# Performance work log

Measured on AMD Instinct MI355X. Metric: run time of the kernel, lower is better.

The kernel has to match this reference:

```python
import jax, jax.numpy as jnp
import numpy as np
from jax import lax

H = 64          # GRU hidden size
OUT_STEPS = 20  # output_seq_size


def _maxpool2(x):
    # x: [N, C, H, W] -> 2x2 max pool, stride 2, VALID
    return lax.reduce_window(x, -jnp.inf, lax.max, (1, 1, 2, 2), (1, 1, 2, 2), 'VALID')


def _conv(x, w, b):
    # NCHW / OIHW, VALID, stride 1
    y = lax.conv_general_dilated(x, w, (1, 1), 'VALID',
                                 dimension_numbers=('NCHW', 'OIHW', 'NCHW'))
    return y + b[None, :, None, None]


def _gru_step(h, x, wih, whh, bih, bhh):
    # PyTorch GRU gate order: r, z, n
    gi = x @ wih.T + bih            # [B, 3H]
    gh = h @ whh.T + bhh            # [B, 3H]
    i_r, i_z, i_n = jnp.split(gi, 3, axis=-1)
    h_r, h_z, h_n = jnp.split(gh, 3, axis=-1)
    r = jax.nn.sigmoid(i_r + h_r)
    z = jax.nn.sigmoid(i_z + h_z)
    n = jnp.tanh(i_n + r * h_n)
    return (1.0 - z) * n + z * h


def setup_inputs() -> dict:
    key = jax.random.key(0)
    ks = jax.random.split(key, 20)
    B, T = 1024, 31
    s = 0.1
    return {
        'bbox_seq': jax.random.normal(ks[0], (B, T, 4), jnp.float32),
        'head_seq': jax.random.uniform(ks[1], (B, T, 32, 32), jnp.float32),
        'conv1_w': jax.random.normal(ks[2], (4, 1, 3, 3), jnp.float32) * s,
        'conv1_b': jax.random.normal(ks[3], (4,), jnp.float32) * s,
        'conv2_w': jax.random.normal(ks[4], (10, 4, 3, 3), jnp.float32) * s,
        'conv2_b': jax.random.normal(ks[5], (10,), jnp.float32) * s,
        'fc_w': jax.random.normal(ks[6], (5, 360), jnp.float32) * s,
        'fc_b': jax.random.normal(ks[7], (5,), jnp.float32) * s,
        'enc_wih': jax.random.normal(ks[8], (3 * H, 9), jnp.float32) * s,
        'enc_whh': jax.random.normal(ks[9], (3 * H, H), jnp.float32) * s,
        'enc_bih': jax.random.normal(ks[10], (3 * H,), jnp.float32) * s,
        'enc_bhh': jax.random.normal(ks[11], (3 * H,), jnp.float32) * s,
        'dec_wih': jax.random.normal(ks[12], (3 * H, 4), jnp.float32) * s,
        'dec_whh': jax.random.normal(ks[13], (3 * H, H), jnp.float32) * s,
        'dec_bih': jax.random.normal(ks[14], (3 * H,), jnp.float32) * s,
        'dec_bhh': jax.random.normal(ks[15], (3 * H,), jnp.float32) * s,
        'lin_w': jax.random.normal(ks[16], (4, H), jnp.float32) * s,
        'lin_b': jax.random.normal(ks[17], (4,), jnp.float32) * s,
    }


def reference(bbox_seq, head_seq, conv1_w, conv1_b, conv2_w, conv2_b, fc_w, fc_b,
              enc_wih, enc_whh, enc_bih, enc_bhh,
              dec_wih, dec_whh, dec_bih, dec_bhh, lin_w, lin_b):
    B, T = bbox_seq.shape[0], bbox_seq.shape[1]
    L = T - 1  # encoder sequence length

    # offset: last bbox, broadcast over OUT_STEPS -> [B, OUT_STEPS, 4]
    offset = jnp.broadcast_to(bbox_seq[:, -1][:, None, :], (B, OUT_STEPS, 4))

    diffs = bbox_seq[:, 1:] - bbox_seq[:, :-1]  # [B, L, 4] (dropout p=0 -> identity)

    # --- ConvEncoder on all head crops at once ---
    imgs = head_seq[:, :-1].reshape(B * L, 1, 32, 32)
    x = jax.nn.relu(_conv(imgs, conv1_w, conv1_b))   # [BL, 4, 30, 30]
    x = _maxpool2(x)                                  # [BL, 4, 15, 15]
    x = jax.nn.relu(_conv(x, conv2_w, conv2_b))       # [BL, 10, 13, 13]
    x = _maxpool2(x)                                  # [BL, 10, 6, 6]
    emb = x.reshape(B * L, -1) @ fc_w.T + fc_b        # [BL, 5]
    emb = emb.reshape(B, L, -1)

    enc_in = jnp.concatenate([diffs, emb], axis=2)    # [B, L, 9]

    # --- GRU encoder (scan over time) ---
    def enc_step(h, x_t):
        h = _gru_step(h, x_t, enc_wih, enc_whh, enc_bih, enc_bhh)
        return h, None
    h0 = jnp.zeros((B, H), enc_in.dtype)
    hn, _ = lax.scan(enc_step, h0, jnp.swapaxes(enc_in, 0, 1))

    def dec_step(carry, _):
        h, prev_x = carry
        h = _gru_step(h, prev_x, dec_wih, dec_whh, dec_bih, dec_bhh)
        x_new = h @ lin_w.T + lin_b + prev_x
        return (h, x_new), x_new
    (_, _), outs = lax.scan(dec_step, (hn, diffs[:, -1]), None, length=OUT_STEPS)
    out = jnp.swapaxes(outs, 0, 1)                    # [B, OUT_STEPS, 4]

    return jnp.cumsum(out, axis=1) + offset
```

## Files before the change

kernel.cpp:

```cpp
#include <hip/hip_runtime.h>
#include <hip/hip_bf16.h>


#define B_    1024
#define L_    30
#define H_    64

__device__ __forceinline__ float sigmoid_f(float v) {
    return 1.f / (1.f + __expf(-v));
}
__device__ __forceinline__ float tanh_f(float v) {
    v = fminf(fmaxf(v, -15.f), 15.f);
    float e = __expf(2.f * v);
    return (e - 1.f) / (e + 1.f);
}
__device__ __forceinline__ void load4_lds(float* r, const float* p) {
    float2 a = *(const float2*)p;
    float2 b = *(const float2*)(p + 2);
    r[0] = a.x; r[1] = a.y; r[2] = b.x; r[3] = b.y;
}

__global__ __launch_bounds__(64) void conv_embed_kernel(
    const float* __restrict__ bbox,
    const float* __restrict__ head,
    const float* __restrict__ c1w, const float* __restrict__ c1b,
    const float* __restrict__ c2w, const float* __restrict__ c2b,
    const float* __restrict__ fcw, const float* __restrict__ fcb,
    float* __restrict__ enc_in)
{
    const int img = blockIdx.x;
    const int b = img / L_;
    const int l = img % L_;
    const int tid = threadIdx.x;

    __shared__ float s_img[32 * 32];
    __shared__ float s_p1[4 * 15 * 16];
    __shared__ float s_p2[360];
    __shared__ float s_red[60];

    {
        const float4* src = (const float4*)(head + ((size_t)b * 31 + (size_t)l) * 1024);
        float4* dst = (float4*)s_img;
        #pragma unroll
        for (int i = 0; i < 4; ++i) dst[tid + 64 * i] = src[tid + 64 * i];
    }
    __syncthreads();

    if (tid < 60) {
        const int c = tid / 15, px = tid % 15;
        const int x0 = 2 * px;
        float w[9];
        #pragma unroll
        for (int k = 0; k < 9; ++k) w[k] = c1w[c * 9 + k];
        const float bias = c1b[c];

        float r0[4], r1[4], r2[4], r3[4];
        load4_lds(r0, s_img + 0 * 32 + x0);
        load4_lds(r1, s_img + 1 * 32 + x0);
        #pragma unroll
        for (int py = 0; py < 15; ++py) {
            load4_lds(r2, s_img + (2 * py + 2) * 32 + x0);
            load4_lds(r3, s_img + (2 * py + 3) * 32 + x0);
            float a00 = bias, a01 = bias, a10 = bias, a11 = bias;
            #pragma unroll
            for (int kx = 0; kx < 3; ++kx) {
                const float w0 = w[kx], w1 = w[3 + kx], w2 = w[6 + kx];
                a00 = fmaf(w0, r0[kx],     fmaf(w1, r1[kx],     fmaf(w2, r2[kx],     a00)));
                a01 = fmaf(w0, r0[kx + 1], fmaf(w1, r1[kx + 1], fmaf(w2, r2[kx + 1], a01)));
                a10 = fmaf(w0, r1[kx],     fmaf(w1, r2[kx],     fmaf(w2, r3[kx],     a10)));
                a11 = fmaf(w0, r1[kx + 1], fmaf(w1, r2[kx + 1], fmaf(w2, r3[kx + 1], a11)));
            }
            a00 = fmaxf(a00, 0.f); a01 = fmaxf(a01, 0.f);
            a10 = fmaxf(a10, 0.f); a11 = fmaxf(a11, 0.f);
            s_p1[c * 240 + py * 16 + px] = fmaxf(fmaxf(a00, a01), fmaxf(a10, a11));
            #pragma unroll
            for (int q = 0; q < 4; ++q) { r0[q] = r2[q]; r1[q] = r3[q]; }
        }
    }
    __syncthreads();

    if (tid < 60) {
        const int c = tid / 6, px = tid % 6;
        const int x0 = 2 * px;
        float w[4][9];
        #pragma unroll
        for (int ic = 0; ic < 4; ++ic)
            #pragma unroll
            for (int k = 0; k < 9; ++k) w[ic][k] = c2w[(c * 4 + ic) * 9 + k];
        const float bias = c2b[c];

        float win[4][4][4];
        #pragma unroll
        for (int ic = 0; ic < 4; ++ic) {
            load4_lds(win[0][ic], s_p1 + ic * 240 + 0 * 16 + x0);
            load4_lds(win[1][ic], s_p1 + ic * 240 + 1 * 16 + x0);
        }
        #pragma unroll
        for (int py = 0; py < 6; ++py) {
            #pragma unroll
            for (int ic = 0; ic < 4; ++ic) {
                load4_lds(win[2][ic], s_p1 + ic * 240 + (2 * py + 2) * 16 + x0);
                load4_lds(win[3][ic], s_p1 + ic * 240 + (2 * py + 3) * 16 + x0);
            }
            float a00 = bias, a01 = bias, a10 = bias, a11 = bias;
            #pragma unroll
            for (int ic = 0; ic < 4; ++ic) {
                #pragma unroll
                for (int kx = 0; kx < 3; ++kx) {
                    const float w0 = w[ic][kx], w1 = w[ic][3 + kx], w2 = w[ic][6 + kx];
                    a00 = fmaf(w0, win[0][ic][kx],     fmaf(w1, win[1][ic][kx],     fmaf(w2, win[2][ic][kx],     a00)));
                    a01 = fmaf(w0, win[0][ic][kx + 1], fmaf(w1, win[1][ic][kx + 1], fmaf(w2, win[2][ic][kx + 1], a01)));
                    a10 = fmaf(w0, win[1][ic][kx],     fmaf(w1, win[2][ic][kx],     fmaf(w2, win[3][ic][kx],     a10)));
                    a11 = fmaf(w0, win[1][ic][kx + 1], fmaf(w1, win[2][ic][kx + 1], fmaf(w2, win[3][ic][kx + 1], a11)));
                }
            }
            a00 = fmaxf(a00, 0.f); a01 = fmaxf(a01, 0.f);
            a10 = fmaxf(a10, 0.f); a11 = fmaxf(a11, 0.f);
            s_p2[c * 36 + py * 6 + px] = fmaxf(fmaxf(a00, a01), fmaxf(a10, a11));
            #pragma unroll
            for (int ic = 0; ic < 4; ++ic)
                #pragma unroll
                for (int q = 0; q < 4; ++q) { win[0][ic][q] = win[2][ic][q]; win[1][ic][q] = win[3][ic][q]; }
        }
    }
    __syncthreads();

    if (tid < 60) {
        const int o = tid / 12, i0 = tid % 12;
        const float* wrow = fcw + o * 360;
        float acc = 0.f;
        #pragma unroll
        for (int k = 0; k < 30; ++k) {
            const int i = i0 + 12 * k;
            acc = fmaf(wrow[i], s_p2[i], acc);
        }
        s_red[tid] = acc;
    }
    __syncthreads();

    float* dst = enc_in + ((size_t)b * L_ + l) * 9;
    if (tid < 5) {
        float acc = fcb[tid];
        #pragma unroll
        for (int k = 0; k < 12; ++k) acc += s_red[tid * 12 + k];
        dst[4 + tid] = acc;
    } else if (tid >= 8 && tid < 12) {
        const int d = tid - 8;
        const float* bb = bbox + (size_t)b * 124 + (size_t)l * 4;
        dst[d] = bb[4 + d] - bb[d];
    }
}

__global__ __launch_bounds__(256) void gru_enc_kernel(
    const float* __restrict__ enc_in,
    const float* __restrict__ wih,
    const float* __restrict__ whh,
    const float* __restrict__ bih,
    const float* __restrict__ bhh,
    float* __restrict__ hn)
{
    const int b = blockIdx.x;
    const int tid = threadIdx.x;
    const int w = tid >> 6, j = tid & 63;

    float Wh[3][16];
    #pragma unroll
    for (int g = 0; g < 3; ++g) {
        const float* row = whh + (g * 64 + j) * 64 + w * 16;
        #pragma unroll
        for (int k = 0; k < 16; ++k) Wh[g][k] = row[k];
    }
    float Wi[3][9];
    #pragma unroll
    for (int g = 0; g < 3; ++g) {
        const float* row = wih + (g * 64 + j) * 9;
        #pragma unroll
        for (int k = 0; k < 9; ++k) Wi[g][k] = row[k];
    }
    const float bi0 = bih[j], bi1 = bih[64 + j], bi2 = bih[128 + j];
    const float bh0 = bhh[j], bh1 = bhh[64 + j], bh2 = bhh[128 + j];

    __shared__ float sp[2][4][3][64];
    float h = 0.f;
    const float* xp = enc_in + (size_t)b * (L_ * 9);

    for (int t = 0; t < L_; ++t) {
        const int pb = t & 1;
        float pr = 0.f, pz = 0.f, pn = 0.f;
        #pragma unroll
        for (int k = 0; k < 16; ++k) {
            const float hk = __shfl(h, w * 16 + k);
            pr = fmaf(Wh[0][k], hk, pr);
            pz = fmaf(Wh[1][k], hk, pz);
            pn = fmaf(Wh[2][k], hk, pn);
        }
        sp[pb][w][0][j] = pr;
        sp[pb][w][1][j] = pz;
        sp[pb][w][2][j] = pn;

        float x[9];
        #pragma unroll
        for (int k = 0; k < 9; ++k) x[k] = xp[t * 9 + k];
        float gr = bi0 + bh0, gz = bi1 + bh1, gni = bi2, gnh = bh2;
        #pragma unroll
        for (int k = 0; k < 9; ++k) {
            gr  = fmaf(Wi[0][k], x[k], gr);
            gz  = fmaf(Wi[1][k], x[k], gz);
            gni = fmaf(Wi[2][k], x[k], gni);
        }
        __syncthreads();
        #pragma unroll
        for (int ww = 0; ww < 4; ++ww) {
            gr  += sp[pb][ww][0][j];
            gz  += sp[pb][ww][1][j];
            gnh += sp[pb][ww][2][j];
        }
        const float r = sigmoid_f(gr);
        const float z = sigmoid_f(gz);
        const float n = tanh_f(gni + r * gnh);
        h = (1.f - z) * n + z * h;
    }
    if (w == 0) hn[(size_t)b * H_ + j] = h;
}

__global__ __launch_bounds__(256) void gru_dec_kernel(
    const float* __restrict__ bbox,
    const float* __restrict__ hn,
    const float* __restrict__ wih,
    const float* __restrict__ whh,
    const float* __restrict__ bih,
    const float* __restrict__ bhh,
    const float* __restrict__ linw,
    const float* __restrict__ linb,
    float* __restrict__ out)
{
    const int b = blockIdx.x;
    const int tid = threadIdx.x;
    const int w = tid >> 6, j = tid & 63;

    float Wh[3][16];
    #pragma unroll
    for (int g = 0; g < 3; ++g) {
        const float* row = whh + (g * 64 + j) * 64 + w * 16;
        #pragma unroll
        for (int k = 0; k < 16; ++k) Wh[g][k] = row[k];
    }
    float Wi[3][4];
    #pragma unroll
    for (int g = 0; g < 3; ++g) {
        const float* row = wih + (g * 64 + j) * 4;
        #pragma unroll
        for (int k = 0; k < 4; ++k) Wi[g][k] = row[k];
    }
    const float bi0 = bih[j], bi1 = bih[64 + j], bi2 = bih[128 + j];
    const float bh0 = bhh[j], bh1 = bhh[64 + j], bh2 = bhh[128 + j];
    const float lw0 = linw[j], lw1 = linw[64 + j], lw2 = linw[128 + j], lw3 = linw[192 + j];
    const float lb0 = linb[0], lb1 = linb[1], lb2 = linb[2], lb3 = linb[3];

    float h = hn[(size_t)b * H_ + j];
    const float* bb = bbox + (size_t)b * 124;
    float px0 = bb[120] - bb[116];
    float px1 = bb[121] - bb[117];
    float px2 = bb[122] - bb[118];
    float px3 = bb[123] - bb[119];
    const float of0 = bb[120], of1 = bb[121], of2 = bb[122], of3 = bb[123];
    float cs0 = 0.f, cs1 = 0.f, cs2 = 0.f, cs3 = 0.f;

    __shared__ float sp[2][4][3][64];
    float* outp = out + (size_t)b * 80;

    for (int t = 0; t < 20; ++t) {
        const int pb = t & 1;
        float pr = 0.f, pz = 0.f, pn = 0.f;
        #pragma unroll
        for (int k = 0; k < 16; ++k) {
            const float hk = __shfl(h, w * 16 + k);
            pr = fmaf(Wh[0][k], hk, pr);
            pz = fmaf(Wh[1][k], hk, pz);
            pn = fmaf(Wh[2][k], hk, pn);
        }
        sp[pb][w][0][j] = pr;
        sp[pb][w][1][j] = pz;
        sp[pb][w][2][j] = pn;

        float gr = bi0 + bh0, gz = bi1 + bh1, gni = bi2, gnh = bh2;
        gr  = fmaf(Wi[0][0], px0, fmaf(Wi[0][1], px1, fmaf(Wi[0][2], px2, fmaf(Wi[0][3], px3, gr))));
        gz  = fmaf(Wi[1][0], px0, fmaf(Wi[1][1], px1, fmaf(Wi[1][2], px2, fmaf(Wi[1][3], px3, gz))));
        gni = fmaf(Wi[2][0], px0, fmaf(Wi[2][1], px1, fmaf(Wi[2][2], px2, fmaf(Wi[2][3], px3, gni))));

        __syncthreads();
        #pragma unroll
        for (int ww = 0; ww < 4; ++ww) {
            gr  += sp[pb][ww][0][j];
            gz  += sp[pb][ww][1][j];
            gnh += sp[pb][ww][2][j];
        }
        const float r = sigmoid_f(gr);
        const float z = sigmoid_f(gz);
        const float n = tanh_f(gni + r * gnh);
        h = (1.f - z) * n + z * h;

        float v0 = lw0 * h, v1 = lw1 * h, v2 = lw2 * h, v3 = lw3 * h;
        #pragma unroll
        for (int s = 32; s > 0; s >>= 1) {
            v0 += __shfl_xor(v0, s);
            v1 += __shfl_xor(v1, s);
            v2 += __shfl_xor(v2, s);
            v3 += __shfl_xor(v3, s);
        }
        px0 = v0 + lb0 + px0;
        px1 = v1 + lb1 + px1;
        px2 = v2 + lb2 + px2;
        px3 = v3 + lb3 + px3;
        cs0 += px0; cs1 += px1; cs2 += px2; cs3 += px3;
        if (tid == 0) {
            outp[t * 4 + 0] = cs0 + of0;
            outp[t * 4 + 1] = cs1 + of1;
            outp[t * 4 + 2] = cs2 + of2;
            outp[t * 4 + 3] = cs3 + of3;
        }
    }
}

extern "C" void kernel_launch(void* const* d_in, const int* in_sizes, int n_in,
                              void* d_out, int out_size, void* d_ws, size_t ws_size,
                              hipStream_t stream) {
    (void)in_sizes; (void)n_in; (void)out_size; (void)ws_size;
    const float* bbox = (const float*)d_in[0];
    const float* head = (const float*)d_in[1];
    const float* c1w  = (const float*)d_in[2];
    const float* c1b  = (const float*)d_in[3];
    const float* c2w  = (const float*)d_in[4];
    const float* c2b  = (const float*)d_in[5];
    const float* fcw  = (const float*)d_in[6];
    const float* fcb  = (const float*)d_in[7];
    const float* ewih = (const float*)d_in[8];
    const float* ewhh = (const float*)d_in[9];
    const float* ebih = (const float*)d_in[10];
    const float* ebhh = (const float*)d_in[11];
    const float* dwih = (const float*)d_in[12];
    const float* dwhh = (const float*)d_in[13];
    const float* dbih = (const float*)d_in[14];
    const float* dbhh = (const float*)d_in[15];
    const float* linw = (const float*)d_in[16];
    const float* linb = (const float*)d_in[17];
    float* out = (float*)d_out;

    float* enc_in = (float*)d_ws;
    float* hn     = enc_in + (size_t)B_ * L_ * 9;

    conv_embed_kernel<<<B_ * L_, 64, 0, stream>>>(bbox, head, c1w, c1b, c2w, c2b,
                                                  fcw, fcb, enc_in);
    gru_enc_kernel<<<B_, 256, 0, stream>>>(enc_in, ewih, ewhh, ebih, ebhh, hn);
    gru_dec_kernel<<<B_, 256, 0, stream>>>(bbox, hn, dwih, dwhh, dbih, dbhh,
                                           linw, linb, out);
}
```

Measured before the change: 341.4 us.

## Fuse GRU encoder and decoder into single-wave kernel with readlane broadcast

Merges the encoder and decoder GRU kernels into one 64-thread-per-sequence kernel. Each lane holds a full 3x64 slice of the recurrent weights in registers and broadcasts h with readlane instead of splitting the dot product across four waves and reducing through shared memory with barriers. This removes the per-step __syncthreads and LDS partial sums, the hn round trip through global memory, and one kernel launch. In exchange it needs about 192+ weight registers per lane, which risks spilling and low occupancy, and each step's serial FMA chain is four times longer.

```diff
diff --git a/kernel.cpp b/kernel.cpp
--- a/kernel.cpp
+++ b/kernel.cpp
@@ -13,6 +13,9 @@
     v = fminf(fmaxf(v, -15.f), 15.f);
     float e = __expf(2.f * v);
     return (e - 1.f) / (e + 1.f);
+}
+__device__ __forceinline__ float bcast(float v, int lane) {
+    return __int_as_float(__builtin_amdgcn_readlane(__float_as_int(v), lane));
 }
 __device__ __forceinline__ void load4_lds(float* r, const float* p) {
     float2 a = *(const float2*)p;
@@ -151,173 +154,129 @@
     }
 }
 
-__global__ __launch_bounds__(256) void gru_enc_kernel(
+__global__ __launch_bounds__(64, 1) void gru_encdec_kernel(
+    const float* __restrict__ bbox,
     const float* __restrict__ enc_in,
-    const float* __restrict__ wih,
-    const float* __restrict__ whh,
-    const float* __restrict__ bih,
-    const float* __restrict__ bhh,
-    float* __restrict__ hn)
-{
-    const int b = blockIdx.x;
-    const int tid = threadIdx.x;
-    const int w = tid >> 6, j = tid & 63;
-
-    float Wh[3][16];
-    #pragma unroll
-    for (int g = 0; g < 3; ++g) {
-        const float* row = whh + (g * 64 + j) * 64 + w * 16;
-        #pragma unroll
-        for (int k = 0; k < 16; ++k) Wh[g][k] = row[k];
-    }
-    float Wi[3][9];
-    #pragma unroll
-    for (int g = 0; g < 3; ++g) {
-        const float* row = wih + (g * 64 + j) * 9;
-        #pragma unroll
-        for (int k = 0; k < 9; ++k) Wi[g][k] = row[k];
-    }
-    const float bi0 = bih[j], bi1 = bih[64 + j], bi2 = bih[128 + j];
-    const float bh0 = bhh[j], bh1 = bhh[64 + j], bh2 = bhh[128 + j];
-
-    __shared__ float sp[2][4][3][64];
-    float h = 0.f;
-    const float* xp = enc_in + (size_t)b * (L_ * 9);
-
-    for (int t = 0; t < L_; ++t) {
-        const int pb = t & 1;
-        float pr = 0.f, pz = 0.f, pn = 0.f;
-        #pragma unroll
-        for (int k = 0; k < 16; ++k) {
-            const float hk = __shfl(h, w * 16 + k);
-            pr = fmaf(Wh[0][k], hk, pr);
-            pz = fmaf(Wh[1][k], hk, pz);
-            pn = fmaf(Wh[2][k], hk, pn);
-        }
-        sp[pb][w][0][j] = pr;
-        sp[pb][w][1][j] = pz;
-        sp[pb][w][2][j] = pn;
-
-        float x[9];
-        #pragma unroll
-        for (int k = 0; k < 9; ++k) x[k] = xp[t * 9 + k];
-        float gr = bi0 + bh0, gz = bi1 + bh1, gni = bi2, gnh = bh2;
-        #pragma unroll
-        for (int k = 0; k < 9; ++k) {
-            gr  = fmaf(Wi[0][k], x[k], gr);
-            gz  = fmaf(Wi[1][k], x[k], gz);
-            gni = fmaf(Wi[2][k], x[k], gni);
-        }
-        __syncthreads();
-        #pragma unroll
-        for (int ww = 0; ww < 4; ++ww) {
-            gr  += sp[pb][ww][0][j];
-            gz  += sp[pb][ww][1][j];
-            gnh += sp[pb][ww][2][j];
-        }
-        const float r = sigmoid_f(gr);
-        const float z = sigmoid_f(gz);
-        const float n = tanh_f(gni + r * gnh);
-        h = (1.f - z) * n + z * h;
-    }
-    if (w == 0) hn[(size_t)b * H_ + j] = h;
-}
-
-__global__ __launch_bounds__(256) void gru_dec_kernel(
-    const float* __restrict__ bbox,
-    const float* __restrict__ hn,
-    const float* __restrict__ wih,
-    const float* __restrict__ whh,
-    const float* __restrict__ bih,
-    const float* __restrict__ bhh,
-    const float* __restrict__ linw,
-    const float* __restrict__ linb,
+    const float* __restrict__ ewih, const float* __restrict__ ewhh,
+    const float* __restrict__ ebih, const float* __restrict__ ebhh,
+    const float* __restrict__ dwih, const float* __restrict__ dwhh,
+    const float* __restrict__ dbih, const float* __restrict__ dbhh,
+    const float* __restrict__ linw, const float* __restrict__ linb,
     float* __restrict__ out)
 {
     const int b = blockIdx.x;
-    const int tid = threadIdx.x;
-    const int w = tid >> 6, j = tid & 63;
-
-    float Wh[3][16];
-    #pragma unroll
-    for (int g = 0; g < 3; ++g) {
-        const float* row = whh + (g * 64 + j) * 64 + w * 16;
-        #pragma unroll
-        for (int k = 0; k < 16; ++k) Wh[g][k] = row[k];
-    }
-    float Wi[3][4];
-    #pragma unroll
-    for (int g = 0; g < 3; ++g) {
-        const float* row = wih + (g * 64 + j) * 4;
-        #pragma unroll
-        for (int k = 0; k < 4; ++k) Wi[g][k] = row[k];
-    }
-    const float bi0 = bih[j], bi1 = bih[64 + j], bi2 = bih[128 + j];
-    const float bh0 = bhh[j], bh1 = bhh[64 + j], bh2 = bhh[128 + j];
-    const float lw0 = linw[j], lw1 = linw[64 + j], lw2 = linw[128 + j], lw3 = linw[192 + j];
-    const float lb0 = linb[0], lb1 = linb[1], lb2 = linb[2], lb3 = linb[3];
-
-    float h = hn[(size_t)b * H_ + j];
-    const float* bb = bbox + (size_t)b * 124;
-    float px0 = bb[120] - bb[116];
-    float px1 = bb[121] - bb[117];
-    float px2 = bb[122] - bb[118];
-    float px3 = bb[123] - bb[119];
-    const float of0 = bb[120], of1 = bb[121], of2 = bb[122], of3 = bb[123];
-    float cs0 = 0.f, cs1 = 0.f, cs2 = 0.f, cs3 = 0.f;
-
-    __shared__ float sp[2][4][3][64];
-    float* outp = out + (size_t)b * 80;
-
-    for (int t = 0; t < 20; ++t) {
-        const int pb = t & 1;
-        float pr = 0.f, pz = 0.f, pn = 0.f;
-        #pragma unroll
-        for (int k = 0; k < 16; ++k) {
-            const float hk = __shfl(h, w * 16 + k);
-            pr = fmaf(Wh[0][k], hk, pr);
-            pz = fmaf(Wh[1][k], hk, pz);
-            pn = fmaf(Wh[2][k], hk, pn);
-        }
-        sp[pb][w][0][j] = pr;
-        sp[pb][w][1][j] = pz;
-        sp[pb][w][2][j] = pn;
-
-        float gr = bi0 + bh0, gz = bi1 + bh1, gni = bi2, gnh = bh2;
-        gr  = fmaf(Wi[0][0], px0, fmaf(Wi[0][1], px1, fmaf(Wi[0][2], px2, fmaf(Wi[0][3], px3, gr))));
-        gz  = fmaf(Wi[1][0], px0, fmaf(Wi[1][1], px1, fmaf(Wi[1][2], px2, fmaf(Wi[1][3], px3, gz))));
-        gni = fmaf(Wi[2][0], px0, fmaf(Wi[2][1], px1, fmaf(Wi[2][2], px2, fmaf(Wi[2][3], px3, gni))));
+    const int j = threadIdx.x;
+
+    __shared__ float xs[272];
+    for (int i = j; i < 270; i += 64) xs[i] = enc_in[(size_t)b * 270 + i];
+
+    float h = 0.f;
+
+    {
+        float Wh[3][64];
+        #pragma unroll
+        for (int g = 0; g < 3; ++g) {
+            const float4* row = (const float4*)(ewhh + (size_t)(g * 64 + j) * 64);
+            #pragma unroll
+            for (int k4 = 0; k4 < 16; ++k4) *(float4*)&Wh[g][4 * k4] = row[k4];
+        }
+        float Wi[3][9];
+        #pragma unroll
+        for (int g = 0; g < 3; ++g) {
+            const float* row = ewih + (g * 64 + j) * 9;
+            #pragma unroll
+            for (int k = 0; k < 9; ++k) Wi[g][k] = row[k];
+        }
+        const float bi0 = ebih[j], bi1 = ebih[64 + j], bi2 = ebih[128 + j];
+        const float bh0 = ebhh[j], bh1 = ebhh[64 + j], bh2 = ebhh[128 + j];
 
         __syncthreads();
-        #pragma unroll
-        for (int ww = 0; ww < 4; ++ww) {
-            gr  += sp[pb][ww][0][j];
-            gz  += sp[pb][ww][1][j];
-            gnh += sp[pb][ww][2][j];
-        }
-        const float r = sigmoid_f(gr);
-        const float z = sigmoid_f(gz);
-        const float n = tanh_f(gni + r * gnh);
-        h = (1.f - z) * n + z * h;
-
-        float v0 = lw0 * h, v1 = lw1 * h, v2 = lw2 * h, v3 = lw3 * h;
-        #pragma unroll
-        for (int s = 32; s > 0; s >>= 1) {
-            v0 += __shfl_xor(v0, s);
-            v1 += __shfl_xor(v1, s);
-            v2 += __shfl_xor(v2, s);
-            v3 += __shfl_xor(v3, s);
-        }
-        px0 = v0 + lb0 + px0;
-        px1 = v1 + lb1 + px1;
-        px2 = v2 + lb2 + px2;
-        px3 = v3 + lb3 + px3;
-        cs0 += px0; cs1 += px1; cs2 += px2; cs3 += px3;
-        if (tid == 0) {
-            outp[t * 4 + 0] = cs0 + of0;
-            outp[t * 4 + 1] = cs1 + of1;
-            outp[t * 4 + 2] = cs2 + of2;
-            outp[t * 4 + 3] = cs3 + of3;
+
+        #pragma unroll 1
+        for (int t = 0; t < L_; ++t) {
+            float gr = bi0 + bh0, gz = bi1 + bh1, gni = bi2, gnh = bh2;
+            #pragma unroll
+            for (int k = 0; k < 9; ++k) {
+                const float xk = xs[t * 9 + k];
+                gr  = fmaf(Wi[0][k], xk, gr);
+                gz  = fmaf(Wi[1][k], xk, gz);
+                gni = fmaf(Wi[2][k], xk, gni);
+            }
+            #pragma unroll
+            for (int k = 0; k < 64; ++k) {
+                const float hk = bcast(h, k);
+                gr  = fmaf(Wh[0][k], hk, gr);
+                gz  = fmaf(Wh[1][k], hk, gz);
+                gnh = fmaf(Wh[2][k], hk, gnh);
+            }
+            const float r = sigmoid_f(gr);
+            const float z = sigmoid_f(gz);
+            const float n = tanh_f(gni + r * gnh);
+            h = (1.f - z) * n + z * h;
+        }
+    }
+
+    {
+        float Wh[3][64];
+        #pragma unroll
+        for (int g = 0; g < 3; ++g) {
+            const float4* row = (const float4*)(dwhh + (size_t)(g * 64 + j) * 64);
+            #pragma unroll
+            for (int k4 = 0; k4 < 16; ++k4) *(float4*)&Wh[g][4 * k4] = row[k4];
+        }
+        float Wi[3][4];
+        #pragma unroll
+        for (int g = 0; g < 3; ++g) {
+            const float* row = dwih + (g * 64 + j) * 4;
+            #pragma unroll
+            for (int k = 0; k < 4; ++k) Wi[g][k] = row[k];
+        }
+        const float bi0 = dbih[j], bi1 = dbih[64 + j], bi2 = dbih[128 + j];
+        const float bh0 = dbhh[j], bh1 = dbhh[64 + j], bh2 = dbhh[128 + j];
+        const float lw0 = linw[j], lw1 = linw[64 + j], lw2 = linw[128 + j], lw3 = linw[192 + j];
+        const float lb0 = linb[0], lb1 = linb[1], lb2 = linb[2], lb3 = linb[3];
+
+        const float* bb = bbox + (size_t)b * 124;
+        float px0 = bb[120] - bb[116];
+        float px1 = bb[121] - bb[117];
+        float px2 = bb[122] - bb[118];
+        float px3 = bb[123] - bb[119];
+        const float of0 = bb[120], of1 = bb[121], of2 = bb[122], of3 = bb[123];
+        float cs0 = 0.f, cs1 = 0.f, cs2 = 0.f, cs3 = 0.f;
+        float4* outp = (float4*)(out + (size_t)b * 80);
+
+        #pragma unroll 1
+        for (int t = 0; t < 20; ++t) {
+            float gr = bi0 + bh0, gz = bi1 + bh1, gni = bi2, gnh = bh2;
+            gr  = fmaf(Wi[0][0], px0, fmaf(Wi[0][1], px1, fmaf(Wi[0][2], px2, fmaf(Wi[0][3], px3, gr))));
+            gz  = fmaf(Wi[1][0], px0, fmaf(Wi[1][1], px1, fmaf(Wi[1][2], px2, fmaf(Wi[1][3], px3, gz))));
+            gni = fmaf(Wi[2][0], px0, fmaf(Wi[2][1], px1, fmaf(Wi[2][2], px2, fmaf(Wi[2][3], px3, gni))));
+            #pragma unroll
+            for (int k = 0; k < 64; ++k) {
+                const float hk = bcast(h, k);
+                gr  = fmaf(Wh[0][k], hk, gr);
+                gz  = fmaf(Wh[1][k], hk, gz);
+                gnh = fmaf(Wh[2][k], hk, gnh);
+            }
+            const float r = sigmoid_f(gr);
+            const float z = sigmoid_f(gz);
+            const float n = tanh_f(gni + r * gnh);
+            h = (1.f - z) * n + z * h;
+
+            float v0 = lw0 * h, v1 = lw1 * h, v2 = lw2 * h, v3 = lw3 * h;
+            #pragma unroll
+            for (int s = 32; s > 0; s >>= 1) {
+                v0 += __shfl_xor(v0, s);
+                v1 += __shfl_xor(v1, s);
+                v2 += __shfl_xor(v2, s);
+                v3 += __shfl_xor(v3, s);
+            }
+            px0 = v0 + lb0 + px0;
+            px1 = v1 + lb1 + px1;
+            px2 = v2 + lb2 + px2;
+            px3 = v3 + lb3 + px3;
+            cs0 += px0; cs1 += px1; cs2 += px2; cs3 += px3;
+            if (j == 0) outp[t] = make_float4(cs0 + of0, cs1 + of1, cs2 + of2, cs3 + of3);
         }
     }
 }
@@ -347,11 +306,11 @@
     float* out = (float*)d_out;
 
     float* enc_in = (float*)d_ws;
-    float* hn     = enc_in + (size_t)B_ * L_ * 9;
 
     conv_embed_kernel<<<B_ * L_, 64, 0, stream>>>(bbox, head, c1w, c1b, c2w, c2b,
                                                   fcw, fcb, enc_in);
-    gru_enc_kernel<<<B_, 256, 0, stream>>>(enc_in, ewih, ewhh, ebih, ebhh, hn);
-    gru_dec_kernel<<<B_, 256, 0, stream>>>(bbox, hn, dwih, dwhh, dbih, dbhh,
-                                           linw, linb, out);
-}
+    gru_encdec_kernel<<<B_, 64, 0, stream>>>(bbox, enc_in,
+                                             ewih, ewhh, ebih, ebhh,
+                                             dwih, dwhh, dbih, dbhh,
+                                             linw, linb, out);
+}
```

New measurement: 320.4 us. 6.2% less time.
